# Optimization experiments

Hardware: AMD Instinct MI355X
Metric: run time of the kernel (lower is better)

The kernel has to match this reference:

```python
import jax, jax.numpy as jnp
import numpy as np

B_SZ, L, H, P, G, N, CS = 2, 2048, 32, 64, 1, 128, 256


def _i8(k, shape):
    return jax.random.randint(k, shape, -127, 128, dtype=jnp.int32).astype(jnp.int8)


def setup_inputs() -> dict:
    key = jax.random.key(0)
    k = jax.random.split(key, 7)
    return {
        "x": _i8(k[0], (B_SZ, L, H, P)),          # quantized int8 activations
        "dt": _i8(k[1], (B_SZ, L, H)),
        "B": _i8(k[2], (B_SZ, L, G, N)),
        "C": _i8(k[3], (B_SZ, L, G, N)),
        "q_A_log": _i8(k[4], (H,)),               # int8 quantized A_log
        "q_D": _i8(k[5], (H,)),                   # int8 quantized D (D_has_hdim=False)
        "dt_bias": jax.random.normal(k[6], (H,), jnp.float32) * 0.1,
        "A_log_scale": jnp.float32(0.02),
        "D_scale": jnp.float32(0.01),
        "dt_scale": jnp.float32(0.03),
        "x_scale": jnp.float32(0.05),
        "B_scale": jnp.float32(0.05),
        "C_scale": jnp.float32(0.05),
    }


def _chunk_scan(x, dt, B, C, q_A_log, q_D, dt_bias,
                A_log_scale, D_scale, dt_scale, x_scale, B_scale, C_scale):
    f32 = jnp.float32
    b, l, h, p = x.shape
    g, n = B.shape[2], B.shape[3]
    cs = CS
    nc = l // cs

    # --- inline dequantization (per-tensor scales, nhead/ndim groups == 0) ---
    xf = x.astype(f32) * x_scale                       # (b, l, h, p)
    dtf = jax.nn.softplus(dt.astype(f32) * dt_scale + dt_bias)   # (b, l, h), dt_limit=(0, inf)
    A = -jnp.exp(q_A_log.astype(f32) * A_log_scale)    # (h,)
    Bf = B.astype(f32) * B_scale                       # (b, l, g, n)
    Cf = C.astype(f32) * C_scale

    # --- chunk the sequence ---
    xc = xf.reshape(b, nc, cs, h, p)
    dtc = dtf.reshape(b, nc, cs, h)
    Bc = Bf.reshape(b, nc, cs, g, n)
    Cc = Cf.reshape(b, nc, cs, g, n)
    rep = h // g
    Bh = jnp.repeat(Bc, rep, axis=3)                   # (b, nc, cs, h, n)
    Ch = jnp.repeat(Cc, rep, axis=3)

    dA = dtc * A                                       # (b, nc, cs, h), <= 0
    cum = jnp.cumsum(dA, axis=2)                       # cumulative log-decay within chunk

    # --- per-chunk states: sum_s exp(cum[-1]-cum[s]) * dt[s] * B[s] (x) x[s] ---
    decay_states = jnp.exp(cum[:, :, -1:, :] - cum)    # (b, nc, cs, h)
    states = jnp.einsum('bzlhn,bzlh,bzlhp->bzhpn', Bh, dtc * decay_states, xc)

    # --- inter-chunk recurrence (sequential scan over chunks) ---
    chunk_decay = jnp.exp(cum[:, :, -1, :])            # (b, nc, h)

    def step(carry, inp):
        s_c, d_c = inp                                 # (b, h, p, n), (b, h)
        new = d_c[:, :, None, None] * carry + s_c
        return new, carry                              # emit state entering this chunk

    states_t = jnp.moveaxis(states, 1, 0)              # (nc, b, h, p, n)
    decay_t = jnp.moveaxis(chunk_decay, 1, 0)          # (nc, b, h)
    final_state, prev_states = jax.lax.scan(
        step, jnp.zeros((b, h, p, n), f32), (states_t, decay_t))
    prev_states = jnp.moveaxis(prev_states, 0, 1)      # (b, nc, h, p, n)

    # --- inter-chunk output: C[l] . state_in * exp(cum[l]) ---
    y_inter = jnp.einsum('bzlhn,bzhpn,bzlh->bzlhp', Ch, prev_states, jnp.exp(cum))

    # --- intra-chunk output: causal (C.B) attention with decay weights ---
    cumT = jnp.moveaxis(cum, 3, 2)                     # (b, nc, h, cs)
    diff = cumT[..., :, None] - cumT[..., None, :]     # (b, nc, h, cs, cs): cum[l]-cum[s]
    mask = jnp.tril(jnp.ones((cs, cs), bool))
    decay_m = jnp.exp(jnp.where(mask, diff, -jnp.inf)) # zero above diagonal, no overflow
    scores = (jnp.einsum('bzlhn,bzshn->bzhls', Ch, Bh)
              * decay_m
              * jnp.moveaxis(dtc, 3, 2)[..., None, :])
    y_intra = jnp.einsum('bzhls,bzshp->bzlhp', scores, xc)

    # --- skip connection D * x (per-head D) ---
    Df = q_D.astype(f32) * D_scale                     # (h,)
    y = (y_intra + y_inter).reshape(b, l, h, p) + xf * Df[None, None, :, None]
    return y


def reference(x, dt, B, C, q_A_log, q_D, dt_bias,
              A_log_scale, D_scale, dt_scale, x_scale, B_scale, C_scale):
    return _chunk_scan(x, dt, B, C, q_A_log, q_D, dt_bias,
                       A_log_scale, D_scale, dt_scale, x_scale, B_scale, C_scale)
```

## Files before the change

kernel.cpp:

```cpp
#include <hip/hip_runtime.h>
#include <math.h>

#define BB 2
#define LSEQ 2048
#define H 32
#define PDIM 64
#define NDIM 128
#define CS 256
#define NC 8

typedef _Float16 half8 __attribute__((ext_vector_type(8)));
typedef _Float16 half4 __attribute__((ext_vector_type(4)));
typedef float floatx4 __attribute__((ext_vector_type(4)));


__device__ __forceinline__ int dot4i8(int a, int b, int c) {
#if __has_builtin(__builtin_amdgcn_sdot4)
    return __builtin_amdgcn_sdot4(a, b, c, false);
#else
    c += ((a << 24) >> 24) * ((b << 24) >> 24);
    c += ((a << 16) >> 24) * ((b << 16) >> 24);
    c += ((a << 8) >> 24) * ((b << 8) >> 24);
    c += (a >> 24) * (b >> 24);
    return c;
#endif
}

__global__ __launch_bounds__(256) void kA1(
    const int* __restrict__ Bm, _Float16* __restrict__ Bt16T)
{
    int t = threadIdx.x;
    int slice = blockIdx.x & 15;
    int zz = blockIdx.x >> 4;
    int z = zz & 7, b = zz >> 3;
    int bz = b * NC + z;
    int nm = t & 15, s8l = t >> 4;
    int n16 = slice & 7, s8 = (slice >> 3) * 16 + s8l;
    const int* bp = Bm + (size_t)(b * LSEQ + z * CS + s8 * 8) * NDIM + n16 * 16 + nm;
    half8 v;
#pragma unroll
    for (int j = 0; j < 8; ++j) v[j] = (_Float16)(float)bp[(size_t)j * NDIM];
    *(half8*)(Bt16T + ((size_t)(bz * 8 + n16) * 32 + s8) * 128 + nm * 8) = v;
}

#define P16_STRIDE 4360
__global__ __launch_bounds__(256, 4) void k013A2(
    const int* __restrict__ dt, const int* __restrict__ qA, const float* __restrict__ dt_bias,
    const float* __restrict__ A_scale_p, const float* __restrict__ dt_scale_p,
    const int* __restrict__ xq, const float* __restrict__ xs_p, const float* __restrict__ Bs_p,
    const _Float16* __restrict__ Bt16T,
    float* __restrict__ cum, float* __restrict__ cAg, float* __restrict__ cdecay,
    signed char* __restrict__ x8, _Float16* __restrict__ statesF16,
    const int* __restrict__ Bm, const int* __restrict__ Cm, const float* __restrict__ Cs_p,
    _Float16* __restrict__ CBh, _Float16* __restrict__ C16T)
{
    __shared__ __align__(16) char USH[19488];
    int t = threadIdx.x;
    if (blockIdx.x < 1024) {
        float* cumS   = (float*)USH;
        float* cB     = (float*)(USH + 1024);
        float* wsum   = (float*)(USH + 2048);
        _Float16* xcS = (_Float16*)(USH + 2064);
        int half = blockIdx.x & 1;
        int id = blockIdx.x >> 1;
        int h = id & 31, z = (id >> 5) & 7, b = id >> 8;
        int bz = b * NC + z, bzh = bz * H + h;
        int lane6 = t & 63, w = t >> 6;

        float A = -__expf((float)qA[h] * (*A_scale_p));
        float raw = (float)dt[(size_t)(b * LSEQ + z * CS + t) * H + h];
        float xin = raw * (*dt_scale_p) + dt_bias[h];
        float sp = (xin > 20.f) ? xin : log1pf(__expf(xin));
        float v = sp * A;
#pragma unroll
        for (int off = 1; off < 64; off <<= 1) {
            float u = __shfl_up(v, off, 64);
            if (lane6 >= off) v += u;
        }
        if (lane6 == 63) wsum[w] = v;
        __syncthreads();
        float add = 0.f;
        for (int wv = 0; wv < w; ++wv) add += wsum[wv];
        float cumv = v + add;
        float cl = wsum[0] + wsum[1] + wsum[2] + wsum[3];
        float xs = *xs_p;
        if (half == 0) {
            cum[(size_t)bzh * CS + t] = cumv;
            cAg[(size_t)bzh * CS + t] = sp * xs;
            if (t == 0) cdecay[bzh] = __expf(cl);
        }
        cumS[t] = cumv;
        cB[t] = sp * __expf(cl - cumv) * xs * (*Bs_p);
        __syncthreads();

        int pq = t & 7, srow = t >> 3;
        int p0 = half * 32 + pq * 4;
        const int* xb = xq + ((size_t)(b * LSEQ + z * CS) * H + h) * PDIM + p0;
        signed char* x8b = x8 + ((size_t)(b * LSEQ + z * CS) * H + h) * PDIM + p0;
        int plocal = pq * 4;
        int pbase = (plocal >> 4) * P16_STRIDE + ((plocal & 15) * 8);
        for (int j = 0; j < 8; ++j) {
            int s = j * 32 + srow;
            int4 w4 = *(const int4*)(xb + (size_t)s * (H * PDIM));
            float c = cB[s];
            int sbase = pbase + (s >> 3) * 136 + (s & 7);
            signed char pk[4];
            int xi[4] = {w4.x, w4.y, w4.z, w4.w};
#pragma unroll
            for (int pp = 0; pp < 4; ++pp) {
                xcS[sbase + pp * 8] = (_Float16)((float)xi[pp] * c);
                pk[pp] = (signed char)xi[pp];
            }
            *(int*)(x8b + (size_t)s * (H * PDIM)) = *(int*)pk;
        }
        __syncthreads();

        int m = lane6 & 15, q = lane6 >> 4;
        int p16l = w & 1, ntb = (w >> 1) * 4;
        const _Float16* abase = xcS + p16l * P16_STRIDE + m * 8;
        const _Float16* bbase = Bt16T + (size_t)(bz * 8) * 32 * 128 + m * 8;
        floatx4 acc[4] = {};
        for (int kk = 0; kk < 8; ++kk) {
            if (cl - cumS[kk * 32 + 31] < -30.f) continue;
            int s8k = kk * 4 + q;
            half8 a = *(const half8*)(abase + s8k * 136);
#pragma unroll
            for (int nt = 0; nt < 4; ++nt) {
                half8 bf = *(const half8*)(bbase + ((size_t)(ntb + nt) * 32 + s8k) * 128);
                acc[nt] = __builtin_amdgcn_mfma_f32_16x16x32_f16(a, bf, acc[nt], 0, 0, 0);
            }
        }
        int p16g = half * 2 + p16l;
        _Float16* sb = statesF16 + (size_t)bzh * 8192;
#pragma unroll
        for (int nt = 0; nt < 4; ++nt)
#pragma unroll
            for (int rr = 0; rr < 4; ++rr)
                sb[(size_t)(p16g * 16 + (ntb + nt) * 2 + (m >> 3)) * 128 + (q * 4 + rr) * 8 + (m & 7)] =
                    (_Float16)(acc[nt][rr] * 0.0625f);
        return;
    }
    {
        int (*Bi)[33] = (int(*)[33])USH;
        int (*Ci)[33] = (int(*)[33])(USH + 8448);
        int bid2 = blockIdx.x - 1024;
        int r = bid2 % 26;
        int zz = bid2 / 26;
        int z = zz & 7, b = zz >> 3;
        int bz = b * NC + z;
        if (r < 10) {
            const int LT[10] = {0,1,1,2,2,2,3,3,3,3};
            const int ST[10] = {0,0,1,0,1,2,0,1,2,3};
            int l0 = LT[r] * 64, s0 = ST[r] * 64;
            const int* Bp = Bm + (size_t)(b * LSEQ + z * CS + s0) * NDIM;
            const int* Cp = Cm + (size_t)(b * LSEQ + z * CS + l0) * NDIM;
            for (int i = t; i < 64 * 32; i += 256) {
                int rr = i >> 5, k = i & 31;
                const int* sb = Bp + rr * NDIM + k * 4;
                const int* sc = Cp + rr * NDIM + k * 4;
                Bi[rr][k] = (sb[0] & 255) | ((sb[1] & 255) << 8) | ((sb[2] & 255) << 16) | ((sb[3] & 255) << 24);
                Ci[rr][k] = (sc[0] & 255) | ((sc[1] & 255) << 8) | ((sc[2] & 255) << 16) | ((sc[3] & 255) << 24);
            }
            __syncthreads();
            float cbscale = (*Bs_p) * (*Cs_p);
            int ll = t & 63, lg = t >> 6;
            int acc[16];
#pragma unroll
            for (int i = 0; i < 16; ++i) acc[i] = 0;
            for (int k = 0; k < 32; ++k) {
                int cw = Ci[ll][k];
#pragma unroll
                for (int si = 0; si < 16; ++si)
                    acc[si] = dot4i8(cw, Bi[lg * 16 + si][k], acc[si]);
            }
            int l = l0 + ll;
            int l16 = l >> 4, lm = l & 15;
            int sb8 = (s0 + lg * 16) >> 3;
            _Float16* bp = CBh + ((size_t)(bz * 16 + l16) * 32 + sb8) * 128 + lm * 8;
#pragma unroll
            for (int g = 0; g < 2; ++g) {
                half8 v;
#pragma unroll
                for (int i = 0; i < 8; ++i) v[i] = (_Float16)((float)acc[g * 8 + i] * cbscale);
                *(half8*)(bp + g * 128) = v;
            }
        } else {
            int slice = r - 10;
            int lm = t >> 4, n8 = t & 15;
            const int* cp = Cm + (size_t)(b * LSEQ + z * CS + slice * 16 + lm) * NDIM + n8 * 8;
            int4 c0 = *(const int4*)cp;
            int4 c1 = *(const int4*)(cp + 4);
            half8 v;
            v[0] = (_Float16)(float)c0.x; v[1] = (_Float16)(float)c0.y;
            v[2] = (_Float16)(float)c0.z; v[3] = (_Float16)(float)c0.w;
            v[4] = (_Float16)(float)c1.x; v[5] = (_Float16)(float)c1.y;
            v[6] = (_Float16)(float)c1.z; v[7] = (_Float16)(float)c1.w;
            *(half8*)(C16T + ((size_t)(bz * 16 + slice) * 16 + n8) * 128 + lm * 8) = v;
        }
    }
}

#define XT_PITCH 136
__global__ __launch_bounds__(256, 4) void k56(
    const signed char* __restrict__ x8, const int* __restrict__ qD,
    const float* __restrict__ cum, const float* __restrict__ cAg,
    const float* __restrict__ cdecay,
    const _Float16* __restrict__ CBh, const _Float16* __restrict__ C16T,
    const _Float16* __restrict__ statesF16,
    const float* __restrict__ Cs_p, const float* __restrict__ xs_p, const float* __restrict__ Ds_p,
    float* __restrict__ out)
{
    __shared__ float cumL[CS];
    __shared__ __align__(16) char smem[4 * 32 * XT_PITCH * 2];
    _Float16* xT = (_Float16*)smem;
    float (*ep)[65] = (float(*)[65])smem;
    int t = threadIdx.x;
    int par = blockIdx.x & 1;
    int id = blockIdx.x >> 1;
    int h = id & 31, z = (id >> 5) & 7, b = id >> 8;
    int bz = b * NC + z, bzh = bz * H + h;
    cumL[t] = cum[(size_t)bzh * CS + t];
    float cav = cAg[(size_t)bzh * CS + t];

    {
        const signed char* xrow = x8 + ((size_t)(b * LSEQ + z * CS + t) * H + h) * PDIM;
        int s8 = t >> 3, sj = t & 7;
        int4 r4 = *(const int4*)xrow;
        int4 r5 = *(const int4*)(xrow + 16);
        int4 r6 = *(const int4*)(xrow + 32);
        int4 r7 = *(const int4*)(xrow + 48);
        int words[16] = {r4.x, r4.y, r4.z, r4.w, r5.x, r5.y, r5.z, r5.w,
                         r6.x, r6.y, r6.z, r6.w, r7.x, r7.y, r7.z, r7.w};
#pragma unroll
        for (int wi = 0; wi < 16; ++wi) {
            int wv = words[wi];
#pragma unroll
            for (int bi = 0; bi < 4; ++bi) {
                int p = wi * 4 + bi;
                int val = (wv << (24 - 8 * bi)) >> 24;
                xT[((p >> 4) * 32 + s8) * XT_PITCH + (p & 15) * 8 + sj] =
                    (_Float16)((float)val * cav);
            }
        }
    }
    __syncthreads();

    int w = t >> 6, lane = t & 63, m = lane & 15, q = lane >> 4;
    floatx4 acc[2][4] = {};

    bool interact[2];
#pragma unroll
    for (int jl = 0; jl < 2; ++jl) interact[jl] = (cumL[(4 * par + 8 * jl + w) * 16] > -80.f);
    const _Float16* cbase = C16T + (size_t)bz * 16 * 16 * 128 + m * 8;
    if (z > 0 && (interact[0] || interact[1])) {
        const float* cdb = cdecay + (size_t)b * NC * H + h;
        for (int kk = 0; kk < 4; ++kk) {
            int n8 = kk * 4 + q;
            half8 bf[4] = {};
            float wsc = 1.f;
            for (int u = z - 1; u >= 0; --u) {
                if (wsc < 1e-8f) break;
                _Float16 wh = (_Float16)wsc;
                const _Float16* sfb = statesF16 + ((size_t)((b * NC + u) * H) + h) * 8192 + m * 8;
#pragma unroll
                for (int pt = 0; pt < 4; ++pt) {
                    half8 fr = *(const half8*)(sfb + (pt * 16 + n8) * 128);
                    bf[pt] += fr * wh;
                }
                wsc *= cdb[(size_t)u * H];
            }
#pragma unroll
            for (int jl = 0; jl < 2; ++jl) {
                if (!interact[jl]) continue;
                int l16 = 4 * par + 8 * jl + w;
                half8 ha = *(const half8*)(cbase + ((size_t)l16 * 16 + n8) * 128);
#pragma unroll
                for (int pt = 0; pt < 4; ++pt)
                    acc[jl][pt] = __builtin_amdgcn_mfma_f32_16x16x32_f16(ha, bf[pt], acc[jl][pt], 0, 0, 0);
            }
        }
    }
    float Cs16 = (*Cs_p) * 16.0f;
#pragma unroll
    for (int jl = 0; jl < 2; ++jl)
#pragma unroll
        for (int r = 0; r < 4; ++r) {
            float e = __expf(cumL[(4 * par + 8 * jl + w) * 16 + q * 4 + r]) * Cs16;
#pragma unroll
            for (int pt = 0; pt < 4; ++pt) acc[jl][pt][r] *= e;
        }

    const _Float16* cbtb = CBh + (size_t)bz * 16 * 32 * 128 + m * 8;
    int l16max = 4 * par + 8 + w;
    for (int kk = 0; kk < 8; ++kk) {
        if (l16max < 2 * kk) continue;
        int s8 = kk * 4 + q;
        half8 bf[4];
#pragma unroll
        for (int pt = 0; pt < 4; ++pt)
            bf[pt] = *(const half8*)(xT + (size_t)(pt * 32 + s8) * XT_PITCH + m * 8);
        floatx4 c0 = *(const floatx4*)(&cumL[kk * 32 + q * 8]);
        floatx4 c1 = *(const floatx4*)(&cumL[kk * 32 + q * 8 + 4]);
#pragma unroll
        for (int jl = 0; jl < 2; ++jl) {
            int l16 = 4 * par + 8 * jl + w;
            if (l16 < 2 * kk) continue;
            if (cumL[l16 * 16] - cumL[kk * 32 + 31] < -30.f) continue;
            int lA = l16 * 16 + m;
            float cum_l = cumL[lA];
            half8 cb8 = *(const half8*)(cbtb + ((size_t)l16 * 32 + s8) * 128);
            half8 a;
#pragma unroll
            for (int jj = 0; jj < 8; ++jj) {
                int s = kk * 32 + q * 8 + jj;
                float cls = (jj < 4) ? c0[jj] : c1[jj - 4];
                float wv = (float)cb8[jj] * __expf(cum_l - cls);
                a[jj] = (_Float16)((s <= lA) ? wv : 0.f);
            }
#pragma unroll
            for (int pt = 0; pt < 4; ++pt)
                acc[jl][pt] = __builtin_amdgcn_mfma_f32_16x16x32_f16(a, bf[pt], acc[jl][pt], 0, 0, 0);
        }
    }

    float xsDf = (*xs_p) * ((float)qD[h] * (*Ds_p));
    __syncthreads();
#pragma unroll
    for (int jl = 0; jl < 2; ++jl) {
        int lbase = jl * 64 + w * 16 + q * 4;
#pragma unroll
        for (int r = 0; r < 4; ++r)
#pragma unroll
            for (int pt = 0; pt < 4; ++pt)
                ep[lbase + r][pt * 16 + m] = acc[jl][pt][r];
    }
    __syncthreads();
    {
        int lloc = t >> 1;
        int jl = lloc >> 6, wv = (lloc >> 4) & 3, lm = lloc & 15;
        int l = (4 * par + 8 * jl + wv) * 16 + lm;
        size_t go = ((size_t)(b * LSEQ + z * CS + l) * H + h) * PDIM + (t & 1) * 32;
        const float* er = &ep[lloc][(t & 1) * 32];
        const signed char* xp8 = x8 + go;
#pragma unroll
        for (int it = 0; it < 8; ++it) {
            int xw = *(const int*)(xp8 + it * 4);
            floatx4 vv;
            vv[0] = er[it * 4 + 0] + (float)((xw << 24) >> 24) * xsDf;
            vv[1] = er[it * 4 + 1] + (float)((xw << 16) >> 24) * xsDf;
            vv[2] = er[it * 4 + 2] + (float)((xw << 8) >> 24) * xsDf;
            vv[3] = er[it * 4 + 3] + (float)(xw >> 24) * xsDf;
            *(floatx4*)(out + go + it * 4) = vv;
        }
    }
}

extern "C" void kernel_launch(void* const* d_in, const int* in_sizes, int n_in,
                              void* d_out, int out_size, void* d_ws, size_t ws_size,
                              hipStream_t stream)
{
    const int* xq = (const int*)d_in[0];
    const int* dt = (const int*)d_in[1];
    const int* Bm = (const int*)d_in[2];
    const int* Cm = (const int*)d_in[3];
    const int* qA = (const int*)d_in[4];
    const int* qD = (const int*)d_in[5];
    const float* dt_bias = (const float*)d_in[6];
    const float* A_scale = (const float*)d_in[7];
    const float* D_scale = (const float*)d_in[8];
    const float* dt_scale = (const float*)d_in[9];
    const float* x_scale = (const float*)d_in[10];
    const float* B_scale = (const float*)d_in[11];
    const float* C_scale = (const float*)d_in[12];
    float* out = (float*)d_out;

    char* ws = (char*)d_ws;
    float* cum           = (float*)(ws);
    float* cAg           = (float*)(ws + 524288);
    float* cdecay        = (float*)(ws + 1048576);
    _Float16* CBh        = (_Float16*)(ws + 1050624);
    _Float16* statesF16  = (_Float16*)(ws + 3147776);
    _Float16* Bt16T      = (_Float16*)(ws + 19924992);
    _Float16* C16T       = (_Float16*)(ws + 20973568);
    signed char* x8      = (signed char*)(ws + 22022144);

    kA1<<<dim3(256), dim3(256), 0, stream>>>(Bm, Bt16T);
    k013A2<<<dim3(1440), dim3(256), 0, stream>>>(dt, qA, dt_bias, A_scale, dt_scale,
                                                 xq, x_scale, B_scale, Bt16T,
                                                 cum, cAg, cdecay, x8, statesF16,
                                                 Bm, Cm, C_scale, CBh, C16T);
    k56<<<dim3(1024), dim3(256), 0, stream>>>(x8, qD, cum, cAg, cdecay, CBh, C16T,
                                              statesF16, C_scale, x_scale, D_scale, out);
}
```

Baseline: 148.6 us.

## Merge k56 row-parity blocks into one block per chunk-head, use exp2

Each k56 block now covers all 16 row tiles of a (b,z,h) chunk-head rather than half of them, so the grid drops from 1024 to 512 blocks. This removes the duplicated x transpose/dequant into shared memory, the duplicated cum loads and the duplicated inter-chunk state accumulation across the two parity blocks. The exponentials move to the base-2 hardware exp, with cum prescaled by log2(e) and the skip thresholds rescaled to match. The cost is twice the accumulator registers, the occupancy hint in launch_bounds is dropped, and the epilogue is split into two shared-memory passes, so per-CU occupancy and parallelism go down.

```diff
diff --git a/kernel.cpp b/kernel.cpp
--- a/kernel.cpp
+++ b/kernel.cpp
@@ -23,6 +23,14 @@
     c += ((a << 8) >> 24) * ((b << 8) >> 24);
     c += (a >> 24) * (b >> 24);
     return c;
+#endif
+}
+
+__device__ __forceinline__ float fexp2(float x) {
+#if __has_builtin(__builtin_amdgcn_exp2f)
+    return __builtin_amdgcn_exp2f(x);
+#else
+    return __expf(x * 0.69314718f);
 #endif
 }
 
@@ -201,7 +209,7 @@
 }
 
 #define XT_PITCH 136
-__global__ __launch_bounds__(256, 4) void k56(
+__global__ __launch_bounds__(256) void k56(
     const signed char* __restrict__ x8, const int* __restrict__ qD,
     const float* __restrict__ cum, const float* __restrict__ cAg,
     const float* __restrict__ cdecay,
@@ -215,11 +223,10 @@
     _Float16* xT = (_Float16*)smem;
     float (*ep)[65] = (float(*)[65])smem;
     int t = threadIdx.x;
-    int par = blockIdx.x & 1;
-    int id = blockIdx.x >> 1;
+    int id = blockIdx.x;
     int h = id & 31, z = (id >> 5) & 7, b = id >> 8;
     int bz = b * NC + z, bzh = bz * H + h;
-    cumL[t] = cum[(size_t)bzh * CS + t];
+    cumL[t] = cum[(size_t)bzh * CS + t] * 1.44269504f;
     float cav = cAg[(size_t)bzh * CS + t];
 
     {
@@ -246,13 +253,13 @@
     __syncthreads();
 
     int w = t >> 6, lane = t & 63, m = lane & 15, q = lane >> 4;
-    floatx4 acc[2][4] = {};
-
-    bool interact[2];
-#pragma unroll
-    for (int jl = 0; jl < 2; ++jl) interact[jl] = (cumL[(4 * par + 8 * jl + w) * 16] > -80.f);
+    floatx4 acc[4][4] = {};
+
+    bool interact[4];
+#pragma unroll
+    for (int j = 0; j < 4; ++j) interact[j] = (cumL[(4 * j + w) * 16] > -115.42f);
     const _Float16* cbase = C16T + (size_t)bz * 16 * 16 * 128 + m * 8;
-    if (z > 0 && (interact[0] || interact[1])) {
+    if (z > 0 && (interact[0] || interact[1] || interact[2] || interact[3])) {
         const float* cdb = cdecay + (size_t)b * NC * H + h;
         for (int kk = 0; kk < 4; ++kk) {
             int n8 = kk * 4 + q;
@@ -270,30 +277,31 @@
                 wsc *= cdb[(size_t)u * H];
             }
 #pragma unroll
-            for (int jl = 0; jl < 2; ++jl) {
-                if (!interact[jl]) continue;
-                int l16 = 4 * par + 8 * jl + w;
+            for (int j = 0; j < 4; ++j) {
+                if (!interact[j]) continue;
+                int l16 = 4 * j + w;
                 half8 ha = *(const half8*)(cbase + ((size_t)l16 * 16 + n8) * 128);
 #pragma unroll
                 for (int pt = 0; pt < 4; ++pt)
-                    acc[jl][pt] = __builtin_amdgcn_mfma_f32_16x16x32_f16(ha, bf[pt], acc[jl][pt], 0, 0, 0);
+                    acc[j][pt] = __builtin_amdgcn_mfma_f32_16x16x32_f16(ha, bf[pt], acc[j][pt], 0, 0, 0);
             }
         }
     }
     float Cs16 = (*Cs_p) * 16.0f;
 #pragma unroll
-    for (int jl = 0; jl < 2; ++jl)
+    for (int j = 0; j < 4; ++j)
 #pragma unroll
         for (int r = 0; r < 4; ++r) {
-            float e = __expf(cumL[(4 * par + 8 * jl + w) * 16 + q * 4 + r]) * Cs16;
-#pragma unroll
-            for (int pt = 0; pt < 4; ++pt) acc[jl][pt][r] *= e;
+            float e = fexp2(cumL[(4 * j + w) * 16 + q * 4 + r]) * Cs16;
+#pragma unroll
+            for (int pt = 0; pt < 4; ++pt) acc[j][pt][r] *= e;
         }
 
     const _Float16* cbtb = CBh + (size_t)bz * 16 * 32 * 128 + m * 8;
-    int l16max = 4 * par + 8 + w;
     for (int kk = 0; kk < 8; ++kk) {
-        if (l16max < 2 * kk) continue;
+        int jmin = (2 * kk - w + 3) >> 2;
+        if (jmin < 0) jmin = 0;
+        if (jmin > 3) continue;
         int s8 = kk * 4 + q;
         half8 bf[4];
 #pragma unroll
@@ -302,10 +310,10 @@
         floatx4 c0 = *(const floatx4*)(&cumL[kk * 32 + q * 8]);
         floatx4 c1 = *(const floatx4*)(&cumL[kk * 32 + q * 8 + 4]);
 #pragma unroll
-        for (int jl = 0; jl < 2; ++jl) {
-            int l16 = 4 * par + 8 * jl + w;
-            if (l16 < 2 * kk) continue;
-            if (cumL[l16 * 16] - cumL[kk * 32 + 31] < -30.f) continue;
+        for (int j = 0; j < 4; ++j) {
+            if (j < jmin) continue;
+            int l16 = 4 * j + w;
+            if (cumL[l16 * 16] - cumL[kk * 32 + 31] < -43.28f) continue;
             int lA = l16 * 16 + m;
             float cum_l = cumL[lA];
             half8 cb8 = *(const half8*)(cbtb + ((size_t)l16 * 32 + s8) * 128);
@@ -314,31 +322,32 @@
             for (int jj = 0; jj < 8; ++jj) {
                 int s = kk * 32 + q * 8 + jj;
                 float cls = (jj < 4) ? c0[jj] : c1[jj - 4];
-                float wv = (float)cb8[jj] * __expf(cum_l - cls);
+                float wv = (float)cb8[jj] * fexp2(cum_l - cls);
                 a[jj] = (_Float16)((s <= lA) ? wv : 0.f);
             }
 #pragma unroll
             for (int pt = 0; pt < 4; ++pt)
-                acc[jl][pt] = __builtin_amdgcn_mfma_f32_16x16x32_f16(a, bf[pt], acc[jl][pt], 0, 0, 0);
+                acc[j][pt] = __builtin_amdgcn_mfma_f32_16x16x32_f16(a, bf[pt], acc[j][pt], 0, 0, 0);
         }
     }
 
     float xsDf = (*xs_p) * ((float)qD[h] * (*Ds_p));
     __syncthreads();
 #pragma unroll
-    for (int jl = 0; jl < 2; ++jl) {
-        int lbase = jl * 64 + w * 16 + q * 4;
-#pragma unroll
-        for (int r = 0; r < 4; ++r)
-#pragma unroll
-            for (int pt = 0; pt < 4; ++pt)
-                ep[lbase + r][pt * 16 + m] = acc[jl][pt][r];
-    }
-    __syncthreads();
-    {
+    for (int pass = 0; pass < 2; ++pass) {
+#pragma unroll
+        for (int jj = 0; jj < 2; ++jj) {
+            int j = pass * 2 + jj;
+            int lbase = (((4 * j + w) * 16) & 127) + q * 4;
+#pragma unroll
+            for (int r = 0; r < 4; ++r)
+#pragma unroll
+                for (int pt = 0; pt < 4; ++pt)
+                    ep[lbase + r][pt * 16 + m] = acc[j][pt][r];
+        }
+        __syncthreads();
         int lloc = t >> 1;
-        int jl = lloc >> 6, wv = (lloc >> 4) & 3, lm = lloc & 15;
-        int l = (4 * par + 8 * jl + wv) * 16 + lm;
+        int l = pass * 128 + lloc;
         size_t go = ((size_t)(b * LSEQ + z * CS + l) * H + h) * PDIM + (t & 1) * 32;
         const float* er = &ep[lloc][(t & 1) * 32];
         const signed char* xp8 = x8 + go;
@@ -352,6 +361,7 @@
             vv[3] = er[it * 4 + 3] + (float)(xw >> 24) * xsDf;
             *(floatx4*)(out + go + it * 4) = vv;
         }
+        __syncthreads();
     }
 }
 
@@ -389,6 +399,6 @@
                                                  xq, x_scale, B_scale, Bt16T,
                                                  cum, cAg, cdecay, x8, statesF16,
                                                  Bm, Cm, C_scale, CBh, C16T);
-    k56<<<dim3(1024), dim3(256), 0, stream>>>(x8, qD, cum, cAg, cdecay, CBh, C16T,
-                                              statesF16, C_scale, x_scale, D_scale, out);
-}
+    k56<<<dim3(512), dim3(256), 0, stream>>>(x8, qD, cum, cAg, cdecay, CBh, C16T,
+                                             statesF16, C_scale, x_scale, D_scale, out);
+}
```

Result: slower. 152.1 us (+2.4%).

## Split inter-chunk state accumulation across waves via LDS, use exp2, prefetch x loads

Applied to the files above, without the earlier changes.

In k56, each wave previously rebuilt all of the decayed previous-state B fragments by itself, repeating the same global reads and half8 FMAs in every wave. Now each wave accumulates one quarter (its own n8 slice), writes it to a new shared buffer bfS, and after a barrier all waves read the full fragments from LDS. The cum values are pre-scaled by log2(e) so the exponentials can use the hardware exp2 directly, and the skip thresholds are rescaled to match. The launch-bounds occupancy hint of 4 is dropped, and in the first kernel the x int4 loads are issued before the cumsum so their latency overlaps it. The costs are more LDS use, an extra barrier, and possibly lower occupancy, and the inter-chunk pass now runs even when neither row group interacts.

```diff
diff --git a/kernel.cpp b/kernel.cpp
--- a/kernel.cpp
+++ b/kernel.cpp
@@ -23,6 +23,14 @@
     c += ((a << 8) >> 24) * ((b << 8) >> 24);
     c += (a >> 24) * (b >> 24);
     return c;
+#endif
+}
+
+__device__ __forceinline__ float fexp2(float x) {
+#if __has_builtin(__builtin_amdgcn_exp2f)
+    return __builtin_amdgcn_exp2f(x);
+#else
+    return __expf(x * 0.69314718f);
 #endif
 }
 
@@ -67,6 +75,14 @@
         int bz = b * NC + z, bzh = bz * H + h;
         int lane6 = t & 63, w = t >> 6;
 
+        int pq = t & 7, srow = t >> 3;
+        int p0 = half * 32 + pq * 4;
+        const int* xb = xq + ((size_t)(b * LSEQ + z * CS) * H + h) * PDIM + p0;
+        int4 w4arr[8];
+#pragma unroll
+        for (int j = 0; j < 8; ++j)
+            w4arr[j] = *(const int4*)(xb + (size_t)(j * 32 + srow) * (H * PDIM));
+
         float A = -__expf((float)qA[h] * (*A_scale_p));
         float raw = (float)dt[(size_t)(b * LSEQ + z * CS + t) * H + h];
         float xin = raw * (*dt_scale_p) + dt_bias[h];
@@ -93,15 +109,13 @@
         cB[t] = sp * __expf(cl - cumv) * xs * (*Bs_p);
         __syncthreads();
 
-        int pq = t & 7, srow = t >> 3;
-        int p0 = half * 32 + pq * 4;
-        const int* xb = xq + ((size_t)(b * LSEQ + z * CS) * H + h) * PDIM + p0;
         signed char* x8b = x8 + ((size_t)(b * LSEQ + z * CS) * H + h) * PDIM + p0;
         int plocal = pq * 4;
         int pbase = (plocal >> 4) * P16_STRIDE + ((plocal & 15) * 8);
+#pragma unroll
         for (int j = 0; j < 8; ++j) {
             int s = j * 32 + srow;
-            int4 w4 = *(const int4*)(xb + (size_t)s * (H * PDIM));
+            int4 w4 = w4arr[j];
             float c = cB[s];
             int sbase = pbase + (s >> 3) * 136 + (s & 7);
             signed char pk[4];
@@ -201,7 +215,7 @@
 }
 
 #define XT_PITCH 136
-__global__ __launch_bounds__(256, 4) void k56(
+__global__ __launch_bounds__(256) void k56(
     const signed char* __restrict__ x8, const int* __restrict__ qD,
     const float* __restrict__ cum, const float* __restrict__ cAg,
     const float* __restrict__ cdecay,
@@ -212,6 +226,7 @@
 {
     __shared__ float cumL[CS];
     __shared__ __align__(16) char smem[4 * 32 * XT_PITCH * 2];
+    __shared__ __align__(16) _Float16 bfS[4 * 4 * 64 * 8];
     _Float16* xT = (_Float16*)smem;
     float (*ep)[65] = (float(*)[65])smem;
     int t = threadIdx.x;
@@ -219,8 +234,9 @@
     int id = blockIdx.x >> 1;
     int h = id & 31, z = (id >> 5) & 7, b = id >> 8;
     int bz = b * NC + z, bzh = bz * H + h;
-    cumL[t] = cum[(size_t)bzh * CS + t];
+    cumL[t] = cum[(size_t)bzh * CS + t] * 1.44269504f;
     float cav = cAg[(size_t)bzh * CS + t];
+    int w = t >> 6, lane = t & 63, m = lane & 15, q = lane >> 4;
 
     {
         const signed char* xrow = x8 + ((size_t)(b * LSEQ + z * CS + t) * H + h) * PDIM;
@@ -245,18 +261,17 @@
     }
     __syncthreads();
 
-    int w = t >> 6, lane = t & 63, m = lane & 15, q = lane >> 4;
     floatx4 acc[2][4] = {};
 
     bool interact[2];
 #pragma unroll
-    for (int jl = 0; jl < 2; ++jl) interact[jl] = (cumL[(4 * par + 8 * jl + w) * 16] > -80.f);
+    for (int jl = 0; jl < 2; ++jl) interact[jl] = (cumL[(4 * par + 8 * jl + w) * 16] > -115.42f);
     const _Float16* cbase = C16T + (size_t)bz * 16 * 16 * 128 + m * 8;
-    if (z > 0 && (interact[0] || interact[1])) {
-        const float* cdb = cdecay + (size_t)b * NC * H + h;
-        for (int kk = 0; kk < 4; ++kk) {
-            int n8 = kk * 4 + q;
-            half8 bf[4] = {};
+    if (z > 0) {
+        {
+            int n8b = w * 4 + q;
+            half8 bacc[4] = {};
+            const float* cdb = cdecay + (size_t)b * NC * H + h;
             float wsc = 1.f;
             for (int u = z - 1; u >= 0; --u) {
                 if (wsc < 1e-8f) break;
@@ -264,11 +279,22 @@
                 const _Float16* sfb = statesF16 + ((size_t)((b * NC + u) * H) + h) * 8192 + m * 8;
 #pragma unroll
                 for (int pt = 0; pt < 4; ++pt) {
-                    half8 fr = *(const half8*)(sfb + (pt * 16 + n8) * 128);
-                    bf[pt] += fr * wh;
+                    half8 fr = *(const half8*)(sfb + (pt * 16 + n8b) * 128);
+                    bacc[pt] += fr * wh;
                 }
                 wsc *= cdb[(size_t)u * H];
             }
+#pragma unroll
+            for (int pt = 0; pt < 4; ++pt)
+                *(half8*)(bfS + ((w * 4 + pt) * 64 + lane) * 8) = bacc[pt];
+        }
+        __syncthreads();
+        for (int kk = 0; kk < 4; ++kk) {
+            int n8 = kk * 4 + q;
+            half8 bf[4];
+#pragma unroll
+            for (int pt = 0; pt < 4; ++pt)
+                bf[pt] = *(const half8*)(bfS + ((kk * 4 + pt) * 64 + lane) * 8);
 #pragma unroll
             for (int jl = 0; jl < 2; ++jl) {
                 if (!interact[jl]) continue;
@@ -285,7 +311,7 @@
     for (int jl = 0; jl < 2; ++jl)
 #pragma unroll
         for (int r = 0; r < 4; ++r) {
-            float e = __expf(cumL[(4 * par + 8 * jl + w) * 16 + q * 4 + r]) * Cs16;
+            float e = fexp2(cumL[(4 * par + 8 * jl + w) * 16 + q * 4 + r]) * Cs16;
 #pragma unroll
             for (int pt = 0; pt < 4; ++pt) acc[jl][pt][r] *= e;
         }
@@ -305,7 +331,7 @@
         for (int jl = 0; jl < 2; ++jl) {
             int l16 = 4 * par + 8 * jl + w;
             if (l16 < 2 * kk) continue;
-            if (cumL[l16 * 16] - cumL[kk * 32 + 31] < -30.f) continue;
+            if (cumL[l16 * 16] - cumL[kk * 32 + 31] < -43.28f) continue;
             int lA = l16 * 16 + m;
             float cum_l = cumL[lA];
             half8 cb8 = *(const half8*)(cbtb + ((size_t)l16 * 32 + s8) * 128);
@@ -314,7 +340,7 @@
             for (int jj = 0; jj < 8; ++jj) {
                 int s = kk * 32 + q * 8 + jj;
                 float cls = (jj < 4) ? c0[jj] : c1[jj - 4];
-                float wv = (float)cb8[jj] * __expf(cum_l - cls);
+                float wv = (float)cb8[jj] * fexp2(cum_l - cls);
                 a[jj] = (_Float16)((s <= lA) ? wv : 0.f);
             }
 #pragma unroll
```

Result: no change. 149.2 us (+0.4%).

## Fuse three kernels into one launch with per-block flag dependencies

Applied to the files above, without the earlier changes.

Merges the B-transpose kernel, the state/CB-prep kernel and the output kernel into one 2720-block kernel. Producer blocks publish a magic value to per-block flags in workspace, and consumer blocks spin on exactly the flags they depend on. This removes two kernel launch boundaries and lets later-stage blocks start while unrelated earlier blocks are still running. The flags are never reset between calls, so on repeated calls the waits pass immediately and the ordering guarantee is lost. Forward progress also relies on producer blocks being scheduled before their consumers. The shared buffer grows to 35840 bytes for every block, which may reduce occupancy.

```diff
diff --git a/kernel.cpp b/kernel.cpp
--- a/kernel.cpp
+++ b/kernel.cpp
@@ -8,6 +8,7 @@
 #define NDIM 128
 #define CS 256
 #define NC 8
+#define MAGIC 0x1F2E3D4C
 
 typedef _Float16 half8 __attribute__((ext_vector_type(8)));
 typedef _Float16 half4 __attribute__((ext_vector_type(4)));
@@ -26,43 +27,60 @@
 #endif
 }
 
-__global__ __launch_bounds__(256) void kA1(
-    const int* __restrict__ Bm, _Float16* __restrict__ Bt16T)
-{
-    int t = threadIdx.x;
-    int slice = blockIdx.x & 15;
-    int zz = blockIdx.x >> 4;
-    int z = zz & 7, b = zz >> 3;
-    int bz = b * NC + z;
-    int nm = t & 15, s8l = t >> 4;
-    int n16 = slice & 7, s8 = (slice >> 3) * 16 + s8l;
-    const int* bp = Bm + (size_t)(b * LSEQ + z * CS + s8 * 8) * NDIM + n16 * 16 + nm;
-    half8 v;
-#pragma unroll
-    for (int j = 0; j < 8; ++j) v[j] = (_Float16)(float)bp[(size_t)j * NDIM];
-    *(half8*)(Bt16T + ((size_t)(bz * 8 + n16) * 32 + s8) * 128 + nm * 8) = v;
+__device__ __forceinline__ void spin_eq(const int* p, int magic) {
+    while (__hip_atomic_load(p, __ATOMIC_ACQUIRE, __HIP_MEMORY_SCOPE_AGENT) != magic)
+        __builtin_amdgcn_s_sleep(4);
 }
 
+__device__ __forceinline__ void publish(int* p, int t) {
+    __syncthreads();
+    if (t == 0) {
+        __threadfence();
+        __hip_atomic_store(p, (int)MAGIC, __ATOMIC_RELEASE, __HIP_MEMORY_SCOPE_AGENT);
+    }
+}
+
 #define P16_STRIDE 4360
-__global__ __launch_bounds__(256, 4) void k013A2(
+#define XT_PITCH 136
+__global__ __launch_bounds__(256, 4) void kMega(
     const int* __restrict__ dt, const int* __restrict__ qA, const float* __restrict__ dt_bias,
     const float* __restrict__ A_scale_p, const float* __restrict__ dt_scale_p,
     const int* __restrict__ xq, const float* __restrict__ xs_p, const float* __restrict__ Bs_p,
-    const _Float16* __restrict__ Bt16T,
+    const int* __restrict__ Bm, const int* __restrict__ Cm, const float* __restrict__ Cs_p,
+    const int* __restrict__ qD, const float* __restrict__ Ds_p,
     float* __restrict__ cum, float* __restrict__ cAg, float* __restrict__ cdecay,
     signed char* __restrict__ x8, _Float16* __restrict__ statesF16,
-    const int* __restrict__ Bm, const int* __restrict__ Cm, const float* __restrict__ Cs_p,
-    _Float16* __restrict__ CBh, _Float16* __restrict__ C16T)
+    _Float16* __restrict__ Bt16T, _Float16* __restrict__ CBh, _Float16* __restrict__ C16T,
+    int* __restrict__ fA1, int* __restrict__ f013, int* __restrict__ fA2,
+    float* __restrict__ out)
 {
-    __shared__ __align__(16) char USH[19488];
+    __shared__ __align__(16) char USH[35840];
     int t = threadIdx.x;
-    if (blockIdx.x < 1024) {
+
+    if (blockIdx.x < 256) {
+        int slice = blockIdx.x & 15;
+        int zz = blockIdx.x >> 4;
+        int z = zz & 7, b = zz >> 3;
+        int bz = b * NC + z;
+        int nm = t & 15, s8l = t >> 4;
+        int n16 = slice & 7, s8 = (slice >> 3) * 16 + s8l;
+        const int* bp = Bm + (size_t)(b * LSEQ + z * CS + s8 * 8) * NDIM + n16 * 16 + nm;
+        half8 v;
+#pragma unroll
+        for (int j = 0; j < 8; ++j) v[j] = (_Float16)(float)bp[(size_t)j * NDIM];
+        *(half8*)(Bt16T + ((size_t)(bz * 8 + n16) * 32 + s8) * 128 + nm * 8) = v;
+        publish(&fA1[blockIdx.x], t);
+        return;
+    }
+
+    if (blockIdx.x < 1280) {
+        int kb = blockIdx.x - 256;
         float* cumS   = (float*)USH;
         float* cB     = (float*)(USH + 1024);
         float* wsum   = (float*)(USH + 2048);
         _Float16* xcS = (_Float16*)(USH + 2064);
-        int half = blockIdx.x & 1;
-        int id = blockIdx.x >> 1;
+        int half = kb & 1;
+        int id = kb >> 1;
         int h = id & 31, z = (id >> 5) & 7, b = id >> 8;
         int bz = b * NC + z, bzh = bz * H + h;
         int lane6 = t & 63, w = t >> 6;
@@ -115,6 +133,9 @@
         }
         __syncthreads();
 
+        if (t < 16) spin_eq(&fA1[(bz << 4) | t], MAGIC);
+        __syncthreads();
+
         int m = lane6 & 15, q = lane6 >> 4;
         int p16l = w & 1, ntb = (w >> 1) * 4;
         const _Float16* abase = xcS + p16l * P16_STRIDE + m * 8;
@@ -138,12 +159,14 @@
             for (int rr = 0; rr < 4; ++rr)
                 sb[(size_t)(p16g * 16 + (ntb + nt) * 2 + (m >> 3)) * 128 + (q * 4 + rr) * 8 + (m & 7)] =
                     (_Float16)(acc[nt][rr] * 0.0625f);
+        publish(&f013[kb], t);
         return;
     }
-    {
+
+    if (blockIdx.x < 1696) {
+        int bid2 = blockIdx.x - 1280;
         int (*Bi)[33] = (int(*)[33])USH;
         int (*Ci)[33] = (int(*)[33])(USH + 8448);
-        int bid2 = blockIdx.x - 1024;
         int r = bid2 % 26;
         int zz = bid2 / 26;
         int z = zz & 7, b = zz >> 3;
@@ -197,160 +220,162 @@
             v[6] = (_Float16)(float)c1.z; v[7] = (_Float16)(float)c1.w;
             *(half8*)(C16T + ((size_t)(bz * 16 + slice) * 16 + n8) * 128 + lm * 8) = v;
         }
+        publish(&fA2[bid2], t);
+        return;
     }
-}
-
-#define XT_PITCH 136
-__global__ __launch_bounds__(256, 4) void k56(
-    const signed char* __restrict__ x8, const int* __restrict__ qD,
-    const float* __restrict__ cum, const float* __restrict__ cAg,
-    const float* __restrict__ cdecay,
-    const _Float16* __restrict__ CBh, const _Float16* __restrict__ C16T,
-    const _Float16* __restrict__ statesF16,
-    const float* __restrict__ Cs_p, const float* __restrict__ xs_p, const float* __restrict__ Ds_p,
-    float* __restrict__ out)
-{
-    __shared__ float cumL[CS];
-    __shared__ __align__(16) char smem[4 * 32 * XT_PITCH * 2];
-    _Float16* xT = (_Float16*)smem;
-    float (*ep)[65] = (float(*)[65])smem;
-    int t = threadIdx.x;
-    int par = blockIdx.x & 1;
-    int id = blockIdx.x >> 1;
-    int h = id & 31, z = (id >> 5) & 7, b = id >> 8;
-    int bz = b * NC + z, bzh = bz * H + h;
-    cumL[t] = cum[(size_t)bzh * CS + t];
-    float cav = cAg[(size_t)bzh * CS + t];
 
     {
-        const signed char* xrow = x8 + ((size_t)(b * LSEQ + z * CS + t) * H + h) * PDIM;
-        int s8 = t >> 3, sj = t & 7;
-        int4 r4 = *(const int4*)xrow;
-        int4 r5 = *(const int4*)(xrow + 16);
-        int4 r6 = *(const int4*)(xrow + 32);
-        int4 r7 = *(const int4*)(xrow + 48);
-        int words[16] = {r4.x, r4.y, r4.z, r4.w, r5.x, r5.y, r5.z, r5.w,
-                         r6.x, r6.y, r6.z, r6.w, r7.x, r7.y, r7.z, r7.w};
-#pragma unroll
-        for (int wi = 0; wi < 16; ++wi) {
-            int wv = words[wi];
-#pragma unroll
-            for (int bi = 0; bi < 4; ++bi) {
-                int p = wi * 4 + bi;
-                int val = (wv << (24 - 8 * bi)) >> 24;
-                xT[((p >> 4) * 32 + s8) * XT_PITCH + (p & 15) * 8 + sj] =
-                    (_Float16)((float)val * cav);
-            }
-        }
-    }
-    __syncthreads();
-
-    int w = t >> 6, lane = t & 63, m = lane & 15, q = lane >> 4;
-    floatx4 acc[2][4] = {};
-
-    bool interact[2];
-#pragma unroll
-    for (int jl = 0; jl < 2; ++jl) interact[jl] = (cumL[(4 * par + 8 * jl + w) * 16] > -80.f);
-    const _Float16* cbase = C16T + (size_t)bz * 16 * 16 * 128 + m * 8;
-    if (z > 0 && (interact[0] || interact[1])) {
-        const float* cdb = cdecay + (size_t)b * NC * H + h;
-        for (int kk = 0; kk < 4; ++kk) {
-            int n8 = kk * 4 + q;
-            half8 bf[4] = {};
-            float wsc = 1.f;
-            for (int u = z - 1; u >= 0; --u) {
-                if (wsc < 1e-8f) break;
-                _Float16 wh = (_Float16)wsc;
-                const _Float16* sfb = statesF16 + ((size_t)((b * NC + u) * H) + h) * 8192 + m * 8;
-#pragma unroll
-                for (int pt = 0; pt < 4; ++pt) {
-                    half8 fr = *(const half8*)(sfb + (pt * 16 + n8) * 128);
-                    bf[pt] += fr * wh;
+        int bid3 = blockIdx.x - 1696;
+        int par = bid3 & 1;
+        int id = bid3 >> 1;
+        int h = id & 31, z = (id >> 5) & 7, b = id >> 8;
+        int bz = b * NC + z, bzh = bz * H + h;
+
+        int nf = 2 * (z + 1);
+        if (t < nf) {
+            int u = t >> 1, hf = t & 1;
+            spin_eq(&f013[((((b << 3) | u) << 5 | h) << 1) | hf], MAGIC);
+        } else if (t < nf + 26) {
+            spin_eq(&fA2[bz * 26 + (t - nf)], MAGIC);
+        }
+        __syncthreads();
+
+        float* cumL = (float*)USH;
+        _Float16* xT = (_Float16*)(USH + 1024);
+        float (*ep)[65] = (float(*)[65])(USH + 1024);
+        cumL[t] = cum[(size_t)bzh * CS + t];
+        float cav = cAg[(size_t)bzh * CS + t];
+
+        {
+            const signed char* xrow = x8 + ((size_t)(b * LSEQ + z * CS + t) * H + h) * PDIM;
+            int s8 = t >> 3, sj = t & 7;
+            int4 r4 = *(const int4*)xrow;
+            int4 r5 = *(const int4*)(xrow + 16);
+            int4 r6 = *(const int4*)(xrow + 32);
+            int4 r7 = *(const int4*)(xrow + 48);
+            int words[16] = {r4.x, r4.y, r4.z, r4.w, r5.x, r5.y, r5.z, r5.w,
+                             r6.x, r6.y, r6.z, r6.w, r7.x, r7.y, r7.z, r7.w};
+#pragma unroll
+            for (int wi = 0; wi < 16; ++wi) {
+                int wv = words[wi];
+#pragma unroll
+                for (int bi = 0; bi < 4; ++bi) {
+                    int p = wi * 4 + bi;
+                    int val = (wv << (24 - 8 * bi)) >> 24;
+                    xT[((p >> 4) * 32 + s8) * XT_PITCH + (p & 15) * 8 + sj] =
+                        (_Float16)((float)val * cav);
                 }
-                wsc *= cdb[(size_t)u * H];
-            }
+            }
+        }
+        __syncthreads();
+
+        int w = t >> 6, lane = t & 63, m = lane & 15, q = lane >> 4;
+        floatx4 acc[2][4] = {};
+
+        bool interact[2];
+#pragma unroll
+        for (int jl = 0; jl < 2; ++jl) interact[jl] = (cumL[(4 * par + 8 * jl + w) * 16] > -80.f);
+        const _Float16* cbase = C16T + (size_t)bz * 16 * 16 * 128 + m * 8;
+        if (z > 0 && (interact[0] || interact[1])) {
+            const float* cdb = cdecay + (size_t)b * NC * H + h;
+            for (int kk = 0; kk < 4; ++kk) {
+                int n8 = kk * 4 + q;
+                half8 bf[4] = {};
+                float wsc = 1.f;
+                for (int u = z - 1; u >= 0; --u) {
+                    if (wsc < 1e-8f) break;
+                    _Float16 wh = (_Float16)wsc;
+                    const _Float16* sfb = statesF16 + ((size_t)((b * NC + u) * H) + h) * 8192 + m * 8;
+#pragma unroll
+                    for (int pt = 0; pt < 4; ++pt) {
+                        half8 fr = *(const half8*)(sfb + (pt * 16 + n8) * 128);
+                        bf[pt] += fr * wh;
+                    }
+                    wsc *= cdb[(size_t)u * H];
+                }
+#pragma unroll
+                for (int jl = 0; jl < 2; ++jl) {
+                    if (!interact[jl]) continue;
+                    int l16 = 4 * par + 8 * jl + w;
+                    half8 ha = *(const half8*)(cbase + ((size_t)l16 * 16 + n8) * 128);
+#pragma unroll
+                    for (int pt = 0; pt < 4; ++pt)
+                        acc[jl][pt] = __builtin_amdgcn_mfma_f32_16x16x32_f16(ha, bf[pt], acc[jl][pt], 0, 0, 0);
+                }
+            }
+        }
+        float Cs16 = (*Cs_p) * 16.0f;
+#pragma unroll
+        for (int jl = 0; jl < 2; ++jl)
+#pragma unroll
+            for (int r = 0; r < 4; ++r) {
+                float e = __expf(cumL[(4 * par + 8 * jl + w) * 16 + q * 4 + r]) * Cs16;
+#pragma unroll
+                for (int pt = 0; pt < 4; ++pt) acc[jl][pt][r] *= e;
+            }
+
+        const _Float16* cbtb = CBh + (size_t)bz * 16 * 32 * 128 + m * 8;
+        int l16max = 4 * par + 8 + w;
+        for (int kk = 0; kk < 8; ++kk) {
+            if (l16max < 2 * kk) continue;
+            int s8 = kk * 4 + q;
+            half8 bf[4];
+#pragma unroll
+            for (int pt = 0; pt < 4; ++pt)
+                bf[pt] = *(const half8*)(xT + (size_t)(pt * 32 + s8) * XT_PITCH + m * 8);
+            floatx4 c0 = *(const floatx4*)(&cumL[kk * 32 + q * 8]);
+            floatx4 c1 = *(const floatx4*)(&cumL[kk * 32 + q * 8 + 4]);
 #pragma unroll
             for (int jl = 0; jl < 2; ++jl) {
-                if (!interact[jl]) continue;
                 int l16 = 4 * par + 8 * jl + w;
-                half8 ha = *(const half8*)(cbase + ((size_t)l16 * 16 + n8) * 128);
+                if (l16 < 2 * kk) continue;
+                if (cumL[l16 * 16] - cumL[kk * 32 + 31] < -30.f) continue;
+                int lA = l16 * 16 + m;
+                float cum_l = cumL[lA];
+                half8 cb8 = *(const half8*)(cbtb + ((size_t)l16 * 32 + s8) * 128);
+                half8 a;
+#pragma unroll
+                for (int jj = 0; jj < 8; ++jj) {
+                    int s = kk * 32 + q * 8 + jj;
+                    float cls = (jj < 4) ? c0[jj] : c1[jj - 4];
+                    float wv = (float)cb8[jj] * __expf(cum_l - cls);
+                    a[jj] = (_Float16)((s <= lA) ? wv : 0.f);
+                }
 #pragma unroll
                 for (int pt = 0; pt < 4; ++pt)
-                    acc[jl][pt] = __builtin_amdgcn_mfma_f32_16x16x32_f16(ha, bf[pt], acc[jl][pt], 0, 0, 0);
-            }
-        }
-    }
-    float Cs16 = (*Cs_p) * 16.0f;
-#pragma unroll
-    for (int jl = 0; jl < 2; ++jl)
-#pragma unroll
-        for (int r = 0; r < 4; ++r) {
-            float e = __expf(cumL[(4 * par + 8 * jl + w) * 16 + q * 4 + r]) * Cs16;
-#pragma unroll
-            for (int pt = 0; pt < 4; ++pt) acc[jl][pt][r] *= e;
-        }
-
-    const _Float16* cbtb = CBh + (size_t)bz * 16 * 32 * 128 + m * 8;
-    int l16max = 4 * par + 8 + w;
-    for (int kk = 0; kk < 8; ++kk) {
-        if (l16max < 2 * kk) continue;
-        int s8 = kk * 4 + q;
-        half8 bf[4];
-#pragma unroll
-        for (int pt = 0; pt < 4; ++pt)
-            bf[pt] = *(const half8*)(xT + (size_t)(pt * 32 + s8) * XT_PITCH + m * 8);
-        floatx4 c0 = *(const floatx4*)(&cumL[kk * 32 + q * 8]);
-        floatx4 c1 = *(const floatx4*)(&cumL[kk * 32 + q * 8 + 4]);
+                    acc[jl][pt] = __builtin_amdgcn_mfma_f32_16x16x32_f16(a, bf[pt], acc[jl][pt], 0, 0, 0);
+            }
+        }
+
+        float xsDf = (*xs_p) * ((float)qD[h] * (*Ds_p));
+        __syncthreads();
 #pragma unroll
         for (int jl = 0; jl < 2; ++jl) {
-            int l16 = 4 * par + 8 * jl + w;
-            if (l16 < 2 * kk) continue;
-            if (cumL[l16 * 16] - cumL[kk * 32 + 31] < -30.f) continue;
-            int lA = l16 * 16 + m;
-            float cum_l = cumL[lA];
-            half8 cb8 = *(const half8*)(cbtb + ((size_t)l16 * 32 + s8) * 128);
-            half8 a;
-#pragma unroll
-            for (int jj = 0; jj < 8; ++jj) {
-                int s = kk * 32 + q * 8 + jj;
-                float cls = (jj < 4) ? c0[jj] : c1[jj - 4];
-                float wv = (float)cb8[jj] * __expf(cum_l - cls);
-                a[jj] = (_Float16)((s <= lA) ? wv : 0.f);
-            }
-#pragma unroll
-            for (int pt = 0; pt < 4; ++pt)
-                acc[jl][pt] = __builtin_amdgcn_mfma_f32_16x16x32_f16(a, bf[pt], acc[jl][pt], 0, 0, 0);
-        }
-    }
-
-    float xsDf = (*xs_p) * ((float)qD[h] * (*Ds_p));
-    __syncthreads();
-#pragma unroll
-    for (int jl = 0; jl < 2; ++jl) {
-        int lbase = jl * 64 + w * 16 + q * 4;
-#pragma unroll
-        for (int r = 0; r < 4; ++r)
-#pragma unroll
-            for (int pt = 0; pt < 4; ++pt)
-                ep[lbase + r][pt * 16 + m] = acc[jl][pt][r];
-    }
-    __syncthreads();
-    {
-        int lloc = t >> 1;
-        int jl = lloc >> 6, wv = (lloc >> 4) & 3, lm = lloc & 15;
-        int l = (4 * par + 8 * jl + wv) * 16 + lm;
-        size_t go = ((size_t)(b * LSEQ + z * CS + l) * H + h) * PDIM + (t & 1) * 32;
-        const float* er = &ep[lloc][(t & 1) * 32];
-        const signed char* xp8 = x8 + go;
-#pragma unroll
-        for (int it = 0; it < 8; ++it) {
-            int xw = *(const int*)(xp8 + it * 4);
-            floatx4 vv;
-            vv[0] = er[it * 4 + 0] + (float)((xw << 24) >> 24) * xsDf;
-            vv[1] = er[it * 4 + 1] + (float)((xw << 16) >> 24) * xsDf;
-            vv[2] = er[it * 4 + 2] + (float)((xw << 8) >> 24) * xsDf;
-            vv[3] = er[it * 4 + 3] + (float)(xw >> 24) * xsDf;
-            *(floatx4*)(out + go + it * 4) = vv;
+            int lbase = jl * 64 + w * 16 + q * 4;
+#pragma unroll
+            for (int r = 0; r < 4; ++r)
+#pragma unroll
+                for (int pt = 0; pt < 4; ++pt)
+                    ep[lbase + r][pt * 16 + m] = acc[jl][pt][r];
+        }
+        __syncthreads();
+        {
+            int lloc = t >> 1;
+            int jl = lloc >> 6, wv = (lloc >> 4) & 3, lm = lloc & 15;
+            int l = (4 * par + 8 * jl + wv) * 16 + lm;
+            size_t go = ((size_t)(b * LSEQ + z * CS + l) * H + h) * PDIM + (t & 1) * 32;
+            const float* er = &ep[lloc][(t & 1) * 32];
+            const signed char* xp8 = x8 + go;
+#pragma unroll
+            for (int it = 0; it < 8; ++it) {
+                int xw = *(const int*)(xp8 + it * 4);
+                floatx4 vv;
+                vv[0] = er[it * 4 + 0] + (float)((xw << 24) >> 24) * xsDf;
+                vv[1] = er[it * 4 + 1] + (float)((xw << 16) >> 24) * xsDf;
+                vv[2] = er[it * 4 + 2] + (float)((xw << 8) >> 24) * xsDf;
+                vv[3] = er[it * 4 + 3] + (float)(xw >> 24) * xsDf;
+                *(floatx4*)(out + go + it * 4) = vv;
+            }
         }
     }
 }
@@ -383,12 +408,16 @@
     _Float16* Bt16T      = (_Float16*)(ws + 19924992);
     _Float16* C16T       = (_Float16*)(ws + 20973568);
     signed char* x8      = (signed char*)(ws + 22022144);
-
-    kA1<<<dim3(256), dim3(256), 0, stream>>>(Bm, Bt16T);
-    k013A2<<<dim3(1440), dim3(256), 0, stream>>>(dt, qA, dt_bias, A_scale, dt_scale,
-                                                 xq, x_scale, B_scale, Bt16T,
-                                                 cum, cAg, cdecay, x8, statesF16,
-                                                 Bm, Cm, C_scale, CBh, C16T);
-    k56<<<dim3(1024), dim3(256), 0, stream>>>(x8, qD, cum, cAg, cdecay, CBh, C16T,
-                                              statesF16, C_scale, x_scale, D_scale, out);
+    int* fA1             = (int*)(ws + 30410752);
+    int* f013            = (int*)(ws + 30411776);
+    int* fA2             = (int*)(ws + 30415872);
+
+    kMega<<<dim3(2720), dim3(256), 0, stream>>>(
+        dt, qA, dt_bias, A_scale, dt_scale,
+        xq, x_scale, B_scale,
+        Bm, Cm, C_scale, qD, D_scale,
+        cum, cAg, cdecay, x8, statesF16,
+        Bt16T, CBh, C16T,
+        fA1, f013, fA2,
+        out);
 }
```

Measured after the change: 309.7 us. +108.5%, slower.
